# Kernel optimization log

Hardware: AMD Instinct MI355X
Metric: run time of the kernel (lower is better)

Reference implementation:

```python
import math
import jax, jax.numpy as jnp
import numpy as np

DIM = 256
B, S = 4, 4096

def setup_inputs() -> dict:
    key = jax.random.key(0)
    k1, k2, k3 = jax.random.split(key, 3)
    X = jax.random.normal(k1, (B, S, DIM), dtype=jnp.float32)
    # torch nn.Linear(dim, 3*dim): weight [3*dim, dim], bias [3*dim]
    bound = 1.0 / math.sqrt(DIM)
    W = jax.random.uniform(k2, (3 * DIM, DIM), minval=-bound, maxval=bound, dtype=jnp.float32)
    b = jax.random.uniform(k3, (3 * DIM,), minval=-bound, maxval=bound, dtype=jnp.float32)
    return {"X": X, "W": W, "b": b}

def reference(X, W, b):
    # fused QKV projection: X @ W^T + b -> [B, S, 3*dim]
    QKV = jnp.einsum('bsd,ed->bse', X, W) + b
    Q, K, V = jnp.split(QKV, 3, axis=-1)
    # scaled dot-product attention (naive, full score matrix per original)
    scores = jnp.einsum('bqd,bkd->bqk', Q, K) / math.sqrt(DIM)
    att = jax.nn.softmax(scores, axis=-1)
    return jnp.einsum('bqk,bkd->bqd', att, V)
```

## Files before the change

kernel.cpp:

```cpp
#include <hip/hip_runtime.h>
#include <hip/hip_bf16.h>

#define B_ 4
#define S_ 4096
#define D_ 256

typedef __attribute__((ext_vector_type(8))) short bf16x8;
typedef __attribute__((ext_vector_type(4))) short short4v;
typedef __attribute__((ext_vector_type(4))) float f32x4;
typedef __attribute__((ext_vector_type(16))) float f32x16;

static __device__ __forceinline__ unsigned short f2bf(float f) {
    unsigned int u = __float_as_uint(f);
    u += 0x7fffu + ((u >> 16) & 1u);
    return (unsigned short)(u >> 16);
}
static __device__ __forceinline__ float bf2f(unsigned short h) {
    return __uint_as_float(((unsigned int)h) << 16);
}

static __device__ __forceinline__ void gload16(const void* g, void* l) {
    __builtin_amdgcn_global_load_lds(
        (const __attribute__((address_space(1))) unsigned int*)g,
        (__attribute__((address_space(3))) unsigned int*)l, 16, 0, 0);
}

__global__ __launch_bounds__(256) void qkv_proj(
    const float* __restrict__ X, const float* __restrict__ W,
    const float* __restrict__ bias,
    unsigned short* __restrict__ Qb, unsigned short* __restrict__ Kb,
    unsigned short* __restrict__ Vt)
{
    __shared__ __align__(16) unsigned short As[64 * 64];
    __shared__ __align__(16) unsigned short Bs[64 * 64];

    const int tid  = threadIdx.x;
    const int lane = tid & 63;
    const int wid  = tid >> 6;
    const int wm   = wid >> 1, wn = wid & 1;
    const int c    = lane & 15, q4 = lane >> 4;
    const int gm0  = blockIdx.x * 64;
    const int gn0  = blockIdx.y * 64;
    const int sr   = tid >> 2;
    const int sc   = (tid & 3) * 16;

    f32x4 acc[2][2] = {};

    for (int kt = 0; kt < 4; ++kt) {
        const int k0 = kt * 64;
        {
            const float4* ga = (const float4*)(X + (size_t)(gm0 + sr) * D_ + k0 + sc);
            const float4* gb = (const float4*)(W + (size_t)(gn0 + sr) * D_ + k0 + sc);
            float4 a0 = ga[0], a1 = ga[1], a2 = ga[2], a3 = ga[3];
            float4 b0 = gb[0], b1 = gb[1], b2 = gb[2], b3 = gb[3];
            float af[16] = {a0.x,a0.y,a0.z,a0.w, a1.x,a1.y,a1.z,a1.w,
                            a2.x,a2.y,a2.z,a2.w, a3.x,a3.y,a3.z,a3.w};
            float bf[16] = {b0.x,b0.y,b0.z,b0.w, b1.x,b1.y,b1.z,b1.w,
                            b2.x,b2.y,b2.z,b2.w, b3.x,b3.y,b3.z,b3.w};
            bf16x8 av0, av1, bv0, bv1;
            #pragma unroll
            for (int j = 0; j < 8; ++j) {
                av0[j] = (short)f2bf(af[j]);     av1[j] = (short)f2bf(af[8 + j]);
                bv0[j] = (short)f2bf(bf[j]);     bv1[j] = (short)f2bf(bf[8 + j]);
            }
            const int sw = (sr & 7) << 3;
            *(bf16x8*)&As[sr * 64 + ((sc + 0) ^ sw)] = av0;
            *(bf16x8*)&As[sr * 64 + ((sc + 8) ^ sw)] = av1;
            *(bf16x8*)&Bs[sr * 64 + ((sc + 0) ^ sw)] = bv0;
            *(bf16x8*)&Bs[sr * 64 + ((sc + 8) ^ sw)] = bv1;
        }
        __syncthreads();
        const int sw = (c & 7) << 3;
        #pragma unroll
        for (int kk = 0; kk < 64; kk += 32) {
            bf16x8 afr[2], bfr[2];
            #pragma unroll
            for (int mf = 0; mf < 2; ++mf) {
                const int row = wm * 32 + mf * 16 + c;
                afr[mf] = *(const bf16x8*)&As[row * 64 + ((kk + 8 * q4) ^ sw)];
            }
            #pragma unroll
            for (int nf = 0; nf < 2; ++nf) {
                const int row = wn * 32 + nf * 16 + c;
                bfr[nf] = *(const bf16x8*)&Bs[row * 64 + ((kk + 8 * q4) ^ sw)];
            }
            #pragma unroll
            for (int mf = 0; mf < 2; ++mf)
                #pragma unroll
                for (int nf = 0; nf < 2; ++nf)
                    acc[mf][nf] = __builtin_amdgcn_mfma_f32_16x16x32_bf16(
                        afr[mf], bfr[nf], acc[mf][nf], 0, 0, 0);
        }
        __syncthreads();
    }

    const int b  = gm0 >> 12;
    const int s0 = gm0 & 4095;
    #pragma unroll
    for (int mf = 0; mf < 2; ++mf) {
        #pragma unroll
        for (int nf = 0; nf < 2; ++nf) {
            const int e  = gn0 + wn * 32 + nf * 16 + c;
            const float bv = bias[e];
            const int srow0 = s0 + wm * 32 + mf * 16 + 4 * q4;
            if (e < 256) {
                #pragma unroll
                for (int i = 0; i < 4; ++i)
                    Qb[((size_t)b * S_ + srow0 + i) * D_ + e] =
                        f2bf(acc[mf][nf][i] + bv);
            } else if (e < 512) {
                #pragma unroll
                for (int i = 0; i < 4; ++i)
                    Kb[((size_t)b * S_ + srow0 + i) * D_ + (e - 256)] =
                        f2bf(acc[mf][nf][i] + bv);
            } else {
                short4v pv;
                #pragma unroll
                for (int i = 0; i < 4; ++i)
                    pv[i] = (short)f2bf(acc[mf][nf][i] + bv);
                *(short4v*)&Vt[((size_t)(b * D_ + (e - 512))) * S_ + srow0] = pv;
            }
        }
    }
}

__global__ __launch_bounds__(256, 1) void attn_fwd(
    const unsigned short* __restrict__ Qb, const unsigned short* __restrict__ Kb,
    const unsigned short* __restrict__ Vt, float* __restrict__ Out)
{
    __shared__ __align__(16) char smem[132096];

    const int bid  = blockIdx.x;
    const int xcd  = bid & 7;
    const int tile = (xcd >> 1) * 64 + (bid >> 3) * 2 + (xcd & 1);
    const int gr0  = tile * 64;
    const int b    = gr0 >> 12;

    const int tid  = threadIdx.x;
    const int wid  = tid >> 6, lane = tid & 63;
    const int ql   = lane & 31, hi = lane >> 5;
    const int rg   = wid & 1;
    const int kh   = wid >> 1;
    const float C  = 0.09016844005556021f;
    const float THR = 40.0f;

    bf16x8 qf[16];
    {
        const size_t qrow = (size_t)(gr0 + rg * 32 + ql) * D_ + 8 * hi;
        #pragma unroll
        for (int m = 0; m < 16; ++m)
            qf[m] = *(const bf16x8*)&Qb[qrow + m * 16];
    }

    const unsigned short* Kbb = Kb + (size_t)b * S_ * D_;
    const unsigned short* Vtb = Vt + (size_t)b * D_ * S_;

    const int kb_ = lane >> 5, i5 = lane & 31;
    const unsigned short* kdma = Kbb + (size_t)(wid * 2048 + kb_) * 256;
    const int vh = wid - 2;
    const unsigned short* vdma = Vtb + (size_t)(lane >> 2) * S_ + vh * 2048
                               + (((lane & 3) ^ ((lane >> 3) & 3)) << 3);

    float* Mbuf = (float*)(smem + 131072);
    float* Lbuf = (float*)(smem + 131584);

    f32x16 o[8] = {};
    float m0 = -1.0e30f, l0 = 0.0f;

    if (wid < 2) {
        char* dst = smem + wid * 16384;
        #pragma unroll
        for (int j = 0; j < 16; ++j)
            gload16(kdma + j * 512 + ((i5 ^ ((2 * j + kb_) & 31)) << 3),
                    dst + j * 1024);
    } else {
        char* dst = smem + 32768 + vh * 16384;
        #pragma unroll
        for (int j = 0; j < 16; ++j)
            gload16(vdma + (size_t)j * 16 * S_, dst + j * 1024);
    }
    __builtin_amdgcn_s_waitcnt(0);
    __syncthreads();

    const int NS = 64;
    int p = 0;

    for (int s = 0; s < NS; ++s) {
        const char* Ksb = smem + p * 65536 + kh * 16384;
        const char* Vsb = smem + p * 65536 + 32768 + kh * 16384;

        f32x16 sa = {}, sb = {};
        #pragma unroll
        for (int m = 0; m < 8; ++m) {
            bf16x8 kf = *(const bf16x8*)(Ksb + ql * 512 + ((m * 32 + hi * 16) ^ (ql << 4)));
            sa = __builtin_amdgcn_mfma_f32_32x32x16_bf16(kf, qf[m], sa, 0, 0, 0);
        }
        #pragma unroll
        for (int m = 8; m < 16; ++m) {
            bf16x8 kf = *(const bf16x8*)(Ksb + ql * 512 + ((m * 32 + hi * 16) ^ (ql << 4)));
            sb = __builtin_amdgcn_mfma_f32_32x32x16_bf16(kf, qf[m], sb, 0, 0, 0);
        }
        f32x16 sacc;
        #pragma unroll
        for (int r = 0; r < 16; ++r) sacc[r] = sa[r] + sb[r];

        if (s + 1 < NS) {
            const int kvn = (s + 1) * 32;
            if (wid < 2) {
                char* dst = smem + (p ^ 1) * 65536 + wid * 16384;
                const unsigned short* src0 = kdma + (size_t)kvn * 256;
                #pragma unroll
                for (int j = 0; j < 16; ++j)
                    gload16(src0 + j * 512 + ((i5 ^ ((2 * j + kb_) & 31)) << 3),
                            dst + j * 1024);
            } else {
                char* dst = smem + (p ^ 1) * 65536 + 32768 + vh * 16384;
                const unsigned short* src0 = vdma + kvn;
                #pragma unroll
                for (int j = 0; j < 16; ++j)
                    gload16(src0 + (size_t)j * 16 * S_, dst + j * 1024);
            }
        }

        float t[8];
        #pragma unroll
        for (int r = 0; r < 8; ++r) t[r] = fmaxf(sacc[r], sacc[r + 8]);
        #pragma unroll
        for (int r = 0; r < 4; ++r) t[r] = fmaxf(t[r], t[r + 4]);
        float rmax = fmaxf(fmaxf(t[0], t[1]), fmaxf(t[2], t[3]));
        rmax = fmaxf(rmax, __shfl_xor(rmax, 32));

        if (__any(rmax > m0 + THR)) {
            const float mn = fmaxf(m0, rmax);
            const float corr = exp2f((m0 - mn) * C);
            m0 = mn;
            l0 *= corr;
            #pragma unroll
            for (int r = 0; r < 16; ++r) {
                const int row = (r & 3) + 8 * (r >> 2) + 4 * hi;
                const float cr = __shfl(corr, row);
                #pragma unroll
                for (int ch = 0; ch < 8; ++ch) o[ch][r] *= cr;
            }
        }

        float rsum = 0.f;
        unsigned int pk[8];
        #pragma unroll
        for (int tt = 0; tt < 8; ++tt) {
            const unsigned short u0 = f2bf(exp2f((sacc[2 * tt]     - m0) * C));
            const unsigned short u1 = f2bf(exp2f((sacc[2 * tt + 1] - m0) * C));
            rsum += bf2f(u0) + bf2f(u1);
            pk[tt] = (unsigned int)u0 | ((unsigned int)u1 << 16);
        }
        rsum += __shfl_xor(rsum, 32);
        l0 += rsum;

        unsigned int Ap[8];
        #pragma unroll
        for (int tt = 0; tt < 8; ++tt) Ap[tt] = __shfl_xor(pk[tt], 32);

        union U { unsigned int w[4]; bf16x8 v; };
        U pa0, pa1;
        if (hi == 0) {
            pa0.w[0] = pk[0]; pa0.w[1] = pk[1]; pa0.w[2] = Ap[0]; pa0.w[3] = Ap[1];
            pa1.w[0] = pk[4]; pa1.w[1] = pk[5]; pa1.w[2] = Ap[4]; pa1.w[3] = Ap[5];
        } else {
            pa0.w[0] = Ap[2]; pa0.w[1] = Ap[3]; pa0.w[2] = pk[2]; pa0.w[3] = pk[3];
            pa1.w[0] = Ap[6]; pa1.w[1] = Ap[7]; pa1.w[2] = pk[6]; pa1.w[3] = pk[7];
        }

        const int vsw = ((ql >> 1) & 3) << 4;
        #pragma unroll
        for (int ch = 0; ch < 8; ++ch) {
            const char* vrow = Vsb + (ch * 32 + ql) * 64;
            bf16x8 vf0 = *(const bf16x8*)(vrow + ((hi * 16)      ^ vsw));
            bf16x8 vf1 = *(const bf16x8*)(vrow + ((hi * 16 + 32) ^ vsw));
            o[ch] = __builtin_amdgcn_mfma_f32_32x32x16_bf16(pa0.v, vf0, o[ch], 0, 0, 0);
            o[ch] = __builtin_amdgcn_mfma_f32_32x32x16_bf16(pa1.v, vf1, o[ch], 0, 0, 0);
        }

        __syncthreads();
        p ^= 1;
    }

    const int qidx = rg * 32 + ql;
    if (hi == 0) Mbuf[qidx * 2 + kh] = m0;
    __syncthreads();

    {
        const float gm = fmaxf(Mbuf[qidx * 2], Mbuf[qidx * 2 + 1]);
        l0 *= exp2f((m0 - gm) * C);
    }
    if (hi == 0) Lbuf[qidx * 2 + kh] = l0;

    float cr[16];
    #pragma unroll
    for (int r = 0; r < 16; ++r) {
        const int row  = (r & 3) + 8 * (r >> 2) + 4 * hi;
        const int ridx = rg * 32 + row;
        const float mw  = Mbuf[ridx * 2 + kh];
        const float gmr = fmaxf(Mbuf[ridx * 2], Mbuf[ridx * 2 + 1]);
        cr[r] = exp2f((mw - gmr) * C);
    }
    #pragma unroll
    for (int ch = 0; ch < 8; ++ch)
        #pragma unroll
        for (int r = 0; r < 16; ++r) o[ch][r] *= cr[r];

    __syncthreads();

    float* Obuf = (float*)smem;
    if (kh == 1) {
        #pragma unroll
        for (int ch = 0; ch < 8; ++ch)
            #pragma unroll
            for (int r = 0; r < 16; ++r) {
                const int row = (r & 3) + 8 * (r >> 2) + 4 * hi;
                Obuf[(rg * 32 + row) * 260 + ch * 32 + ql] = o[ch][r];
            }
    }
    __syncthreads();

    if (kh == 0) {
        #pragma unroll
        for (int r = 0; r < 16; ++r) {
            const int row  = (r & 3) + 8 * (r >> 2) + 4 * hi;
            const int ridx = rg * 32 + row;
            const float inv = 1.0f / (Lbuf[ridx * 2] + Lbuf[ridx * 2 + 1]);
            #pragma unroll
            for (int ch = 0; ch < 8; ++ch)
                Out[(size_t)(gr0 + ridx) * D_ + ch * 32 + ql] =
                    (o[ch][r] + Obuf[ridx * 260 + ch * 32 + ql]) * inv;
        }
    }
}

extern "C" void kernel_launch(void* const* d_in, const int* in_sizes, int n_in,
                              void* d_out, int out_size, void* d_ws, size_t ws_size,
                              hipStream_t stream) {
    (void)out_size; (void)ws_size;
    const void *Xp = nullptr, *Wp = nullptr, *bp = nullptr;
    for (int i = 0; i < n_in; ++i) {
        if      (in_sizes[i] == B_ * S_ * D_) Xp = d_in[i];
        else if (in_sizes[i] == 3 * D_ * D_)  Wp = d_in[i];
        else if (in_sizes[i] == 3 * D_)       bp = d_in[i];
    }
    if (!Xp) Xp = d_in[0];
    if (!Wp) Wp = d_in[1];
    if (!bp) bp = d_in[2];

    float* Out = (float*)d_out;

    unsigned short* Qb = (unsigned short*)d_ws;
    unsigned short* Kb = Qb + (size_t)B_ * S_ * D_;
    unsigned short* Vt = Kb + (size_t)B_ * S_ * D_;

    dim3 pgrid(256, 12);
    qkv_proj<<<pgrid, 256, 0, stream>>>((const float*)Xp, (const float*)Wp,
                                        (const float*)bp, Qb, Kb, Vt);
    attn_fwd<<<256, 256, 0, stream>>>(Qb, Kb, Vt, Out);
}
```

Baseline: 197.2 us.

## Split attention across eight waves using 16x16x32 MFMA tiles

The attention kernel goes from 4 to 8 waves per block, each owning 16 query rows, and switches from 32x32x16 to 16x16x32 bf16 MFMAs. Each lane now holds one query row, so the online-softmax rescale needs no per-row shuffles, and P is packed with v_cvt_pk_bf16_f32. K/V loads are spread across all eight waves and issued at the top of the loop. The aim is better latency hiding and less softmax overhead per wave. The __launch_bounds__(512, 2) hint caps registers per thread, which raises spill risk, while LDS use still allows only one block per CU.

```diff
diff --git a/kernel.cpp b/kernel.cpp
--- a/kernel.cpp
+++ b/kernel.cpp
@@ -8,7 +8,6 @@
 typedef __attribute__((ext_vector_type(8))) short bf16x8;
 typedef __attribute__((ext_vector_type(4))) short short4v;
 typedef __attribute__((ext_vector_type(4))) float f32x4;
-typedef __attribute__((ext_vector_type(16))) float f32x16;
 
 static __device__ __forceinline__ unsigned short f2bf(float f) {
     unsigned int u = __float_as_uint(f);
@@ -17,6 +16,11 @@
 }
 static __device__ __forceinline__ float bf2f(unsigned short h) {
     return __uint_as_float(((unsigned int)h) << 16);
+}
+static __device__ __forceinline__ unsigned int cvtpk(float lo, float hi) {
+    unsigned int r;
+    asm("v_cvt_pk_bf16_f32 %0, %1, %2" : "=v"(r) : "v"(lo), "v"(hi));
+    return r;
 }
 
 static __device__ __forceinline__ void gload16(const void* g, void* l) {
@@ -124,7 +128,7 @@
     }
 }
 
-__global__ __launch_bounds__(256, 1) void attn_fwd(
+__global__ __launch_bounds__(512, 2) void attn_fwd(
     const unsigned short* __restrict__ Qb, const unsigned short* __restrict__ Kb,
     const unsigned short* __restrict__ Vt, float* __restrict__ Out)
 {
@@ -138,96 +142,94 @@
 
     const int tid  = threadIdx.x;
     const int wid  = tid >> 6, lane = tid & 63;
-    const int ql   = lane & 31, hi = lane >> 5;
-    const int rg   = wid & 1;
-    const int kh   = wid >> 1;
+    const int qi   = lane & 15, g = lane >> 4;
+    const int rg   = wid & 3;
+    const int kh   = wid >> 2;
+    const int q0   = gr0 + rg * 16;
     const float C  = 0.09016844005556021f;
     const float THR = 40.0f;
 
-    bf16x8 qf[16];
+    bf16x8 qf[8];
     {
-        const size_t qrow = (size_t)(gr0 + rg * 32 + ql) * D_ + 8 * hi;
-        #pragma unroll
-        for (int m = 0; m < 16; ++m)
-            qf[m] = *(const bf16x8*)&Qb[qrow + m * 16];
+        const size_t qrow = (size_t)(q0 + qi) * D_ + 8 * g;
+        #pragma unroll
+        for (int m = 0; m < 8; ++m)
+            qf[m] = *(const bf16x8*)&Qb[qrow + m * 32];
     }
 
     const unsigned short* Kbb = Kb + (size_t)b * S_ * D_;
     const unsigned short* Vtb = Vt + (size_t)b * D_ * S_;
 
-    const int kb_ = lane >> 5, i5 = lane & 31;
-    const unsigned short* kdma = Kbb + (size_t)(wid * 2048 + kb_) * 256;
-    const int vh = wid - 2;
-    const unsigned short* vdma = Vtb + (size_t)(lane >> 2) * S_ + vh * 2048
-                               + (((lane & 3) ^ ((lane >> 3) & 3)) << 3);
+    const int isK = (wid < 4);
+    const int sth = (wid >> 1) & 1;
+    const int sub = wid & 1;
+    int soff[8];
+    int doff[8];
+    if (isK) {
+        const int l5 = lane >> 5, i5 = lane & 31;
+        #pragma unroll
+        for (int j = 0; j < 8; ++j) {
+            const int r0 = sub * 16 + 2 * j + l5;
+            soff[j] = (sth * 2048 + r0) * 256 + ((i5 ^ r0) << 3);
+            doff[j] = sth * 16384 + (sub * 16 + 2 * j) * 512;
+        }
+    } else {
+        #pragma unroll
+        for (int j = 0; j < 8; ++j) {
+            const int d = sub * 128 + 16 * j + (lane >> 2);
+            soff[j] = d * S_ + sth * 2048 + ((((lane & 3) ^ ((lane >> 3) & 3))) << 3);
+            doff[j] = 32768 + sth * 16384 + (sub * 128 + 16 * j) * 64;
+        }
+    }
+    const unsigned short* sbase = isK ? Kbb : Vtb;
 
     float* Mbuf = (float*)(smem + 131072);
     float* Lbuf = (float*)(smem + 131584);
 
-    f32x16 o[8] = {};
+    f32x4 o[16] = {};
     float m0 = -1.0e30f, l0 = 0.0f;
 
-    if (wid < 2) {
-        char* dst = smem + wid * 16384;
-        #pragma unroll
-        for (int j = 0; j < 16; ++j)
-            gload16(kdma + j * 512 + ((i5 ^ ((2 * j + kb_) & 31)) << 3),
-                    dst + j * 1024);
-    } else {
-        char* dst = smem + 32768 + vh * 16384;
-        #pragma unroll
-        for (int j = 0; j < 16; ++j)
-            gload16(vdma + (size_t)j * 16 * S_, dst + j * 1024);
-    }
+    #pragma unroll
+    for (int j = 0; j < 8; ++j)
+        gload16(sbase + soff[j], smem + doff[j]);
     __builtin_amdgcn_s_waitcnt(0);
     __syncthreads();
 
     const int NS = 64;
     int p = 0;
+    const int vsw = (g ^ ((qi >> 1) & 3)) << 4;
 
     for (int s = 0; s < NS; ++s) {
+        if (s + 1 < NS) {
+            const unsigned short* sb = sbase + (isK ? (s + 1) * 32 * 256
+                                                    : (s + 1) * 32);
+            const int bufo = (p ^ 1) * 65536;
+            #pragma unroll
+            for (int j = 0; j < 8; ++j)
+                gload16(sb + soff[j], smem + bufo + doff[j]);
+        }
+
         const char* Ksb = smem + p * 65536 + kh * 16384;
         const char* Vsb = smem + p * 65536 + 32768 + kh * 16384;
 
-        f32x16 sa = {}, sb = {};
-        #pragma unroll
-        for (int m = 0; m < 8; ++m) {
-            bf16x8 kf = *(const bf16x8*)(Ksb + ql * 512 + ((m * 32 + hi * 16) ^ (ql << 4)));
-            sa = __builtin_amdgcn_mfma_f32_32x32x16_bf16(kf, qf[m], sa, 0, 0, 0);
-        }
-        #pragma unroll
-        for (int m = 8; m < 16; ++m) {
-            bf16x8 kf = *(const bf16x8*)(Ksb + ql * 512 + ((m * 32 + hi * 16) ^ (ql << 4)));
-            sb = __builtin_amdgcn_mfma_f32_32x32x16_bf16(kf, qf[m], sb, 0, 0, 0);
-        }
-        f32x16 sacc;
-        #pragma unroll
-        for (int r = 0; r < 16; ++r) sacc[r] = sa[r] + sb[r];
-
-        if (s + 1 < NS) {
-            const int kvn = (s + 1) * 32;
-            if (wid < 2) {
-                char* dst = smem + (p ^ 1) * 65536 + wid * 16384;
-                const unsigned short* src0 = kdma + (size_t)kvn * 256;
-                #pragma unroll
-                for (int j = 0; j < 16; ++j)
-                    gload16(src0 + j * 512 + ((i5 ^ ((2 * j + kb_) & 31)) << 3),
-                            dst + j * 1024);
-            } else {
-                char* dst = smem + (p ^ 1) * 65536 + 32768 + vh * 16384;
-                const unsigned short* src0 = vdma + kvn;
-                #pragma unroll
-                for (int j = 0; j < 16; ++j)
-                    gload16(src0 + (size_t)j * 16 * S_, dst + j * 1024);
-            }
-        }
-
-        float t[8];
-        #pragma unroll
-        for (int r = 0; r < 8; ++r) t[r] = fmaxf(sacc[r], sacc[r + 8]);
-        #pragma unroll
-        for (int r = 0; r < 4; ++r) t[r] = fmaxf(t[r], t[r + 4]);
-        float rmax = fmaxf(fmaxf(t[0], t[1]), fmaxf(t[2], t[3]));
+        f32x4 sacc[2] = {};
+        #pragma unroll
+        for (int kc = 0; kc < 2; ++kc) {
+            const int kr = kc * 16 + qi;
+            const char* krow = Ksb + kr * 512;
+            #pragma unroll
+            for (int m = 0; m < 8; ++m) {
+                bf16x8 kf = *(const bf16x8*)(krow + (((4 * m + g) ^ kr) << 4));
+                sacc[kc] = __builtin_amdgcn_mfma_f32_16x16x32_bf16(
+                    kf, qf[m], sacc[kc], 0, 0, 0);
+            }
+        }
+
+        float rmax = fmaxf(fmaxf(fmaxf(sacc[0][0], sacc[0][1]),
+                                 fmaxf(sacc[0][2], sacc[0][3])),
+                           fmaxf(fmaxf(sacc[1][0], sacc[1][1]),
+                                 fmaxf(sacc[1][2], sacc[1][3])));
+        rmax = fmaxf(rmax, __shfl_xor(rmax, 16));
         rmax = fmaxf(rmax, __shfl_xor(rmax, 32));
 
         if (__any(rmax > m0 + THR)) {
@@ -236,103 +238,84 @@
             m0 = mn;
             l0 *= corr;
             #pragma unroll
-            for (int r = 0; r < 16; ++r) {
-                const int row = (r & 3) + 8 * (r >> 2) + 4 * hi;
-                const float cr = __shfl(corr, row);
-                #pragma unroll
-                for (int ch = 0; ch < 8; ++ch) o[ch][r] *= cr;
-            }
-        }
-
+            for (int dc = 0; dc < 16; ++dc)
+                #pragma unroll
+                for (int r = 0; r < 4; ++r) o[dc][r] *= corr;
+        }
+
+        float p8[2][4];
         float rsum = 0.f;
-        unsigned int pk[8];
-        #pragma unroll
-        for (int tt = 0; tt < 8; ++tt) {
-            const unsigned short u0 = f2bf(exp2f((sacc[2 * tt]     - m0) * C));
-            const unsigned short u1 = f2bf(exp2f((sacc[2 * tt + 1] - m0) * C));
-            rsum += bf2f(u0) + bf2f(u1);
-            pk[tt] = (unsigned int)u0 | ((unsigned int)u1 << 16);
-        }
+        #pragma unroll
+        for (int kc = 0; kc < 2; ++kc)
+            #pragma unroll
+            for (int r = 0; r < 4; ++r) {
+                p8[kc][r] = exp2f((sacc[kc][r] - m0) * C);
+                rsum += p8[kc][r];
+            }
+        rsum += __shfl_xor(rsum, 16);
         rsum += __shfl_xor(rsum, 32);
         l0 += rsum;
 
-        unsigned int Ap[8];
-        #pragma unroll
-        for (int tt = 0; tt < 8; ++tt) Ap[tt] = __shfl_xor(pk[tt], 32);
-
-        union U { unsigned int w[4]; bf16x8 v; };
-        U pa0, pa1;
-        if (hi == 0) {
-            pa0.w[0] = pk[0]; pa0.w[1] = pk[1]; pa0.w[2] = Ap[0]; pa0.w[3] = Ap[1];
-            pa1.w[0] = pk[4]; pa1.w[1] = pk[5]; pa1.w[2] = Ap[4]; pa1.w[3] = Ap[5];
-        } else {
-            pa0.w[0] = Ap[2]; pa0.w[1] = Ap[3]; pa0.w[2] = pk[2]; pa0.w[3] = pk[3];
-            pa1.w[0] = Ap[6]; pa1.w[1] = Ap[7]; pa1.w[2] = pk[6]; pa1.w[3] = pk[7];
-        }
-
-        const int vsw = ((ql >> 1) & 3) << 4;
-        #pragma unroll
-        for (int ch = 0; ch < 8; ++ch) {
-            const char* vrow = Vsb + (ch * 32 + ql) * 64;
-            bf16x8 vf0 = *(const bf16x8*)(vrow + ((hi * 16)      ^ vsw));
-            bf16x8 vf1 = *(const bf16x8*)(vrow + ((hi * 16 + 32) ^ vsw));
-            o[ch] = __builtin_amdgcn_mfma_f32_32x32x16_bf16(pa0.v, vf0, o[ch], 0, 0, 0);
-            o[ch] = __builtin_amdgcn_mfma_f32_32x32x16_bf16(pa1.v, vf1, o[ch], 0, 0, 0);
+        unsigned int pk0[2], pk1[2];
+        pk0[0] = cvtpk(p8[0][0], p8[0][1]);  pk0[1] = cvtpk(p8[0][2], p8[0][3]);
+        pk1[0] = cvtpk(p8[1][0], p8[1][1]);  pk1[1] = cvtpk(p8[1][2], p8[1][3]);
+
+        const int A0 = qi + ((g & 1) << 5);
+        const int A1 = A0 + 16;
+        const unsigned int s00 = __shfl(pk0[0], A0), s01 = __shfl(pk0[1], A0);
+        const unsigned int s02 = __shfl(pk0[0], A1), s03 = __shfl(pk0[1], A1);
+        const unsigned int s10 = __shfl(pk1[0], A0), s11 = __shfl(pk1[1], A0);
+        const unsigned int s12 = __shfl(pk1[0], A1), s13 = __shfl(pk1[1], A1);
+        const bool hk = (g >> 1);
+        union U { unsigned int w[4]; bf16x8 v; } pa;
+        pa.w[0] = hk ? s10 : s00;  pa.w[1] = hk ? s11 : s01;
+        pa.w[2] = hk ? s12 : s02;  pa.w[3] = hk ? s13 : s03;
+
+        #pragma unroll
+        for (int dc = 0; dc < 16; ++dc) {
+            bf16x8 vf = *(const bf16x8*)(Vsb + (dc * 16 + qi) * 64 + vsw);
+            o[dc] = __builtin_amdgcn_mfma_f32_16x16x32_bf16(vf, pa.v, o[dc], 0, 0, 0);
         }
 
         __syncthreads();
         p ^= 1;
     }
 
-    const int qidx = rg * 32 + ql;
-    if (hi == 0) Mbuf[qidx * 2 + kh] = m0;
+    const int qidx = rg * 16 + qi;
+    if (g == 0) Mbuf[qidx * 2 + kh] = m0;
     __syncthreads();
 
     {
         const float gm = fmaxf(Mbuf[qidx * 2], Mbuf[qidx * 2 + 1]);
-        l0 *= exp2f((m0 - gm) * C);
-    }
-    if (hi == 0) Lbuf[qidx * 2 + kh] = l0;
-
-    float cr[16];
-    #pragma unroll
-    for (int r = 0; r < 16; ++r) {
-        const int row  = (r & 3) + 8 * (r >> 2) + 4 * hi;
-        const int ridx = rg * 32 + row;
-        const float mw  = Mbuf[ridx * 2 + kh];
-        const float gmr = fmaxf(Mbuf[ridx * 2], Mbuf[ridx * 2 + 1]);
-        cr[r] = exp2f((mw - gmr) * C);
-    }
-    #pragma unroll
-    for (int ch = 0; ch < 8; ++ch)
-        #pragma unroll
-        for (int r = 0; r < 16; ++r) o[ch][r] *= cr[r];
-
-    __syncthreads();
+        const float corr = exp2f((m0 - gm) * C);
+        l0 *= corr;
+        #pragma unroll
+        for (int dc = 0; dc < 16; ++dc)
+            #pragma unroll
+            for (int r = 0; r < 4; ++r) o[dc][r] *= corr;
+    }
+    if (g == 0) Lbuf[qidx * 2 + kh] = l0;
 
     float* Obuf = (float*)smem;
     if (kh == 1) {
         #pragma unroll
-        for (int ch = 0; ch < 8; ++ch)
-            #pragma unroll
-            for (int r = 0; r < 16; ++r) {
-                const int row = (r & 3) + 8 * (r >> 2) + 4 * hi;
-                Obuf[(rg * 32 + row) * 260 + ch * 32 + ql] = o[ch][r];
-            }
+        for (int dc = 0; dc < 16; ++dc)
+            #pragma unroll
+            for (int r = 0; r < 4; ++r)
+                Obuf[qidx * 260 + dc * 16 + 4 * g + r] = o[dc][r];
     }
     __syncthreads();
 
     if (kh == 0) {
-        #pragma unroll
-        for (int r = 0; r < 16; ++r) {
-            const int row  = (r & 3) + 8 * (r >> 2) + 4 * hi;
-            const int ridx = rg * 32 + row;
-            const float inv = 1.0f / (Lbuf[ridx * 2] + Lbuf[ridx * 2 + 1]);
-            #pragma unroll
-            for (int ch = 0; ch < 8; ++ch)
-                Out[(size_t)(gr0 + ridx) * D_ + ch * 32 + ql] =
-                    (o[ch][r] + Obuf[ridx * 260 + ch * 32 + ql]) * inv;
-        }
+        const float inv = 1.0f / (Lbuf[qidx * 2] + Lbuf[qidx * 2 + 1]);
+        #pragma unroll
+        for (int dc = 0; dc < 16; ++dc)
+            #pragma unroll
+            for (int r = 0; r < 4; ++r) {
+                const int d = dc * 16 + 4 * g + r;
+                Out[(size_t)(q0 + qi) * D_ + d] =
+                    (o[dc][r] + Obuf[qidx * 260 + d]) * inv;
+            }
     }
 }
 
@@ -359,5 +342,5 @@
     dim3 pgrid(256, 12);
     qkv_proj<<<pgrid, 256, 0, stream>>>((const float*)Xp, (const float*)Wp,
                                         (const float*)bp, Qb, Kb, Vt);
-    attn_fwd<<<256, 256, 0, stream>>>(Qb, Kb, Vt, Out);
-}
+    attn_fwd<<<256, 512, 0, stream>>>(Qb, Kb, Vt, Out);
+}
```

Result: faster. 161.8 us (-17.9%).
